# Optimization experiments

Measured on AMD Instinct MI355X. Metric: run time of the kernel, lower is better.

The kernel has to match this reference:

```python
import jax, jax.numpy as jnp
import numpy as np

N = 8192
IN_F = 512
OUT_F = 128
NEG_BIG = -9.0e15


def setup_inputs() -> dict:
    key = jax.random.key(0)
    k_x, k_adj, k_w, k_a1, k_a2 = jax.random.split(key, 5)
    X = jax.random.normal(k_x, (N, IN_F), dtype=jnp.float32)
    adj = jax.random.randint(k_adj, (N, N), 0, 2, dtype=jnp.int32)
    # xavier_uniform with gain=1.414
    gain = 1.414
    lim_w = gain * np.sqrt(6.0 / (IN_F + OUT_F))
    W = jax.random.uniform(k_w, (IN_F, OUT_F), minval=-lim_w, maxval=lim_w, dtype=jnp.float32)
    lim_a = gain * np.sqrt(6.0 / (OUT_F + 1))
    a_1 = jax.random.uniform(k_a1, (OUT_F, 1), minval=-lim_a, maxval=lim_a, dtype=jnp.float32)
    a_2 = jax.random.uniform(k_a2, (OUT_F, 1), minval=-lim_a, maxval=lim_a, dtype=jnp.float32)
    return {"X": X, "adj": adj, "W": W, "a_1": a_1, "a_2": a_2}


def reference(X, adj, W, a_1, a_2):
    h = X @ W                         # [N, out]
    Wh1 = h @ a_1                     # [N, 1]
    Wh2 = h @ a_2                     # [N, 1]
    alpha = Wh1 + Wh2.T               # [N, N] broadcast score sum
    s = jax.nn.sigmoid(alpha)
    masked = jnp.where(adj > 0, s, jnp.float32(NEG_BIG))
    attn = jax.nn.softmax(masked, axis=1)  # dropout p=0.0 -> identity
    return attn @ h                   # [N, out]
```

## Files before the change

### kernel.cpp

```cpp
#include <hip/hip_runtime.h>
#include <hip/hip_bf16.h>

#define N_NODES 8192
#define IN_F 512
#define OUT_F 128
#define KSHIFT 3
#define KP (1 << KSHIFT)
#define KT_PER (256 >> KSHIFT)
#define LOG2E 1.4426950408889634f

typedef unsigned short u16;
typedef unsigned int u32;
typedef short s16x8 __attribute__((ext_vector_type(8)));
typedef float f32x4 __attribute__((ext_vector_type(4)));
typedef u32 u32x4 __attribute__((ext_vector_type(4)));

__device__ __forceinline__ u16 f2bf(float f) {
    union { float f; unsigned u; } x; x.f = f;
    unsigned r = x.u + 0x7FFFu + ((x.u >> 16) & 1u);
    return (u16)(r >> 16);
}

__device__ __forceinline__ u32 packbf2(float a, float b) {
    __hip_bfloat162 h = __float22bfloat162_rn(make_float2(a, b));
    u32 u; __builtin_memcpy(&u, &h, 4);
    return u;
}

__device__ __forceinline__ float edge_p(float wh1, float w2, int keep) {
    float alpha = wh1 + w2;
    float e = exp2f(-LOG2E * alpha);
    float s = __builtin_amdgcn_rcpf(1.0f + e);
    float p = exp2f(LOG2E * s);
    return keep ? p : 0.0f;
}

__global__ void repack_W(const float* __restrict__ W, u16* __restrict__ W_frag) {
    int tid = blockIdx.x * 256 + threadIdx.x;
    int j = tid & 7;
    int lane = (tid >> 3) & 63;
    int nt = (tid >> 9) & 7;
    int kt = tid >> 12;
    int k = kt * 32 + (lane >> 4) * 8 + j;
    int n = nt * 16 + (lane & 15);
    W_frag[tid] = f2bf(W[k * OUT_F + n]);
}

__global__ void compute_Wa(const float* __restrict__ W, const float* __restrict__ a1,
                           const float* __restrict__ a2,
                           float* __restrict__ Wa1, float* __restrict__ Wa2) {
    int k = blockIdx.x * 256 + threadIdx.x;
    if (k >= IN_F) return;
    float s1 = 0.f, s2 = 0.f;
    #pragma unroll 8
    for (int n = 0; n < OUT_F; n++) {
        float w = W[k * OUT_F + n];
        s1 += w * a1[n];
        s2 += w * a2[n];
    }
    Wa1[k] = s1; Wa2[k] = s2;
}

__global__ __launch_bounds__(256)
void gemm_h(const float* __restrict__ X, const u16* __restrict__ W_frag,
            const float* __restrict__ Wa1, const float* __restrict__ Wa2,
            float* __restrict__ Wh1, float* __restrict__ Wh2,
            u16* __restrict__ h_frag) {
    int tid = threadIdx.x;
    int wave = tid >> 6;
    int lane = tid & 63;
    int quad = lane >> 4;
    int lid = lane & 15;
    int rbase = blockIdx.x * 16;
    const float* xrow = X + (size_t)(rbase + lid) * IN_F;
    const s16x8* Wf = (const s16x8*)W_frag;
    f32x4 acc0 = {}, acc1 = {};
    float p1 = 0.f, p2 = 0.f;
    int nt0 = wave * 2;

    for (int kt = 0; kt < 16; kt++) {
        int k0 = kt * 32 + quad * 8;
        float4 x0 = *(const float4*)(xrow + k0);
        float4 x1 = *(const float4*)(xrow + k0 + 4);
        u32x4 uv;
        uv.x = packbf2(x0.x, x0.y); uv.y = packbf2(x0.z, x0.w);
        uv.z = packbf2(x1.x, x1.y); uv.w = packbf2(x1.z, x1.w);
        s16x8 a = __builtin_bit_cast(s16x8, uv);
        if (wave == 0) {
            float4 wa = *(const float4*)(Wa1 + k0);
            float4 wb = *(const float4*)(Wa1 + k0 + 4);
            float4 wc = *(const float4*)(Wa2 + k0);
            float4 wd = *(const float4*)(Wa2 + k0 + 4);
        p1 += x0.x*wa.x + x0.y*wa.y + x0.z*wa.z + x0.w*wa.w
            + x1.x*wb.x + x1.y*wb.y + x1.z*wb.z + x1.w*wb.w;
        p2 += x0.x*wc.x + x0.y*wc.y + x0.z*wc.z + x0.w*wc.w
            + x1.x*wd.x + x1.y*wd.y + x1.z*wd.z + x1.w*wd.w;
        }
        s16x8 b0 = Wf[(kt * 8 + nt0) * 64 + lane];
        s16x8 b1 = Wf[(kt * 8 + nt0 + 1) * 64 + lane];
        acc0 = __builtin_amdgcn_mfma_f32_16x16x32_bf16(a, b0, acc0, 0, 0, 0);
        acc1 = __builtin_amdgcn_mfma_f32_16x16x32_bf16(a, b1, acc1, 0, 0, 0);
    }

    #pragma unroll
    for (int reg = 0; reg < 4; reg++) {
        int row = rbase + quad * 4 + reg;
        int ktile = row >> 5, kl = row & 31;
        int lane2 = (kl >> 3) * 16 + lid, j2 = kl & 7;
        h_frag[(size_t)((ktile * 8 + nt0) * 64 + lane2) * 8 + j2] = f2bf(acc0[reg]);
        h_frag[(size_t)((ktile * 8 + nt0 + 1) * 64 + lane2) * 8 + j2] = f2bf(acc1[reg]);
    }
    if (wave == 0) {
        p1 += __shfl_xor(p1, 16, 64); p1 += __shfl_xor(p1, 32, 64);
        p2 += __shfl_xor(p2, 16, 64); p2 += __shfl_xor(p2, 32, 64);
        if (lane < 16) { Wh1[rbase + lid] = p1; Wh2[rbase + lid] = p2; }
    }
}

__global__ __launch_bounds__(256)
void attn_kernel(const int* __restrict__ adj, const float* __restrict__ Wh1,
                 const float* __restrict__ Wh2, const u16* __restrict__ h_frag,
                 float* __restrict__ out_part, float* __restrict__ sum_part) {
    int tid = threadIdx.x;
    int wave = tid >> 6;
    int lane = tid & 63;
    int quad = lane >> 4;
    int lid = lane & 15;
    int rtile = blockIdx.x >> KSHIFT;
    int kh = blockIdx.x & (KP - 1);
    int rbase = rtile * 128 + wave * 32;
    int r0 = rbase + lid, r1 = r0 + 16;

    float wh10 = Wh1[r0], wh11 = Wh1[r1];
    f32x4 acc0[8] = {}, acc1[8] = {};
    float ps0 = 0.f, ps1 = 0.f;
    const s16x8* Hf = (const s16x8*)h_frag;
    const int* adjrow0 = adj + (size_t)r0 * N_NODES;
    const int* adjrow1 = adj + (size_t)r1 * N_NODES;

    const int kt0 = kh * KT_PER;
    #pragma unroll 1
    for (int kt = kt0; kt < kt0 + KT_PER; kt++) {
        int k0 = kt * 32 + quad * 8;
        int4 aj0a = *(const int4*)(adjrow0 + k0);
        int4 aj0b = *(const int4*)(adjrow0 + k0 + 4);
        int4 aj1a = *(const int4*)(adjrow1 + k0);
        int4 aj1b = *(const int4*)(adjrow1 + k0 + 4);
        float4 w20 = *(const float4*)(Wh2 + k0);
        float4 w21 = *(const float4*)(Wh2 + k0 + 4);

        float e0 = edge_p(wh10, w20.x, aj0a.x), e1 = edge_p(wh10, w20.y, aj0a.y);
        float e2 = edge_p(wh10, w20.z, aj0a.z), e3 = edge_p(wh10, w20.w, aj0a.w);
        float e4 = edge_p(wh10, w21.x, aj0b.x), e5 = edge_p(wh10, w21.y, aj0b.y);
        float e6 = edge_p(wh10, w21.z, aj0b.z), e7 = edge_p(wh10, w21.w, aj0b.w);
        ps0 += ((e0 + e1) + (e2 + e3)) + ((e4 + e5) + (e6 + e7));
        u32x4 uv0;
        uv0.x = packbf2(e0, e1); uv0.y = packbf2(e2, e3);
        uv0.z = packbf2(e4, e5); uv0.w = packbf2(e6, e7);

        float f0 = edge_p(wh11, w20.x, aj1a.x), f1 = edge_p(wh11, w20.y, aj1a.y);
        float f2 = edge_p(wh11, w20.z, aj1a.z), f3 = edge_p(wh11, w20.w, aj1a.w);
        float f4 = edge_p(wh11, w21.x, aj1b.x), f5 = edge_p(wh11, w21.y, aj1b.y);
        float f6 = edge_p(wh11, w21.z, aj1b.z), f7 = edge_p(wh11, w21.w, aj1b.w);
        ps1 += ((f0 + f1) + (f2 + f3)) + ((f4 + f5) + (f6 + f7));
        u32x4 uv1;
        uv1.x = packbf2(f0, f1); uv1.y = packbf2(f2, f3);
        uv1.z = packbf2(f4, f5); uv1.w = packbf2(f6, f7);

        s16x8 af0 = __builtin_bit_cast(s16x8, uv0);
        s16x8 af1 = __builtin_bit_cast(s16x8, uv1);

        #pragma unroll
        for (int nt = 0; nt < 8; nt++) {
            s16x8 b = Hf[(kt * 8 + nt) * 64 + lane];
            acc0[nt] = __builtin_amdgcn_mfma_f32_16x16x32_bf16(af0, b, acc0[nt], 0, 0, 0);
            acc1[nt] = __builtin_amdgcn_mfma_f32_16x16x32_bf16(af1, b, acc1[nt], 0, 0, 0);
        }
    }

    ps0 += __shfl_xor(ps0, 16, 64); ps0 += __shfl_xor(ps0, 32, 64);
    ps1 += __shfl_xor(ps1, 16, 64); ps1 += __shfl_xor(ps1, 32, 64);
    if (quad == 0) {
        sum_part[(size_t)kh * N_NODES + r0] = ps0;
        sum_part[(size_t)kh * N_NODES + r1] = ps1;
    }

    #pragma unroll
    for (int nt = 0; nt < 8; nt++) {
        #pragma unroll
        for (int reg = 0; reg < 4; reg++) {
            int row0 = rbase + quad * 4 + reg;
            int col = nt * 16 + lid;
            out_part[((size_t)kh * N_NODES + row0) * OUT_F + col] = acc0[nt][reg];
            out_part[((size_t)kh * N_NODES + row0 + 16) * OUT_F + col] = acc1[nt][reg];
        }
    }
}

__global__ void finalize(const float* __restrict__ out_part,
                         const float* __restrict__ sum_part,
                         float* __restrict__ out) {
    int gid = blockIdx.x * 256 + threadIdx.x;
    int i = gid >> 7;
    float s = 0.f, v = 0.f;
    for (int kh = 0; kh < KP; kh++) {
        s += sum_part[(size_t)kh * N_NODES + i];
        v += out_part[(size_t)kh * N_NODES * OUT_F + gid];
    }
    out[gid] = v / s;
}

extern "C" void kernel_launch(void* const* d_in, const int* in_sizes, int n_in,
                              void* d_out, int out_size, void* d_ws, size_t ws_size,
                              hipStream_t stream) {
    const float* X   = (const float*)d_in[0];
    const int*   adj = (const int*)d_in[1];
    const float* W   = (const float*)d_in[2];
    const float* a1  = (const float*)d_in[3];
    const float* a2  = (const float*)d_in[4];

    const size_t BASE = (size_t)4 << 20;
    char* ws = (char*)d_ws;
    float* Wh1 = (float*)(ws);
    float* Wh2 = (float*)(ws + (32 << 10));
    float* Wa1 = (float*)(ws + (64 << 10));
    float* Wa2 = (float*)(ws + (66 << 10));
    u16* W_frag = (u16*)(ws + (128 << 10));
    u16* h_frag = (u16*)(ws + (256 << 10));
    float* out_part = (float*)(ws + BASE);
    float* sum_part = (float*)(ws + BASE + ((size_t)KP << 22));
    float* out = (float*)d_out;

    hipLaunchKernelGGL(repack_W, dim3(256), dim3(256), 0, stream, W, W_frag);
    hipLaunchKernelGGL(compute_Wa, dim3(2), dim3(256), 0, stream, W, a1, a2, Wa1, Wa2);
    hipLaunchKernelGGL(gemm_h, dim3(512), dim3(256), 0, stream,
                       X, W_frag, Wa1, Wa2, Wh1, Wh2, h_frag);
    hipLaunchKernelGGL(attn_kernel, dim3(64 * KP), dim3(256), 0, stream,
                       adj, Wh1, Wh2, h_frag, out_part, sum_part);
    hipLaunchKernelGGL(finalize, dim3((N_NODES * OUT_F) / 256), dim3(256), 0, stream,
                       out_part, sum_part, out);
}
```

Before: 438.0 us.

## Stage h tiles in LDS, prefetch adjacency two steps ahead, double K split

The attention kernel now loads each group of four k-tiles of h fragments into shared memory once per block, so the four waves no longer each fetch them from global memory. It also software-prefetches the adjacency int4 loads two iterations ahead into register double buffers. The K split doubles, giving twice as many blocks with shorter loops. The price is more partial outputs to write and reduce, extra barriers, and higher register pressure.

```diff
diff --git a/kernel.cpp b/kernel.cpp
--- a/kernel.cpp
+++ b/kernel.cpp
@@ -4,7 +4,7 @@
 #define N_NODES 8192
 #define IN_F 512
 #define OUT_F 128
-#define KSHIFT 3
+#define KSHIFT 4
 #define KP (1 << KSHIFT)
 #define KT_PER (256 >> KSHIFT)
 #define LOG2E 1.4426950408889634f
@@ -91,10 +91,10 @@
             float4 wb = *(const float4*)(Wa1 + k0 + 4);
             float4 wc = *(const float4*)(Wa2 + k0);
             float4 wd = *(const float4*)(Wa2 + k0 + 4);
-        p1 += x0.x*wa.x + x0.y*wa.y + x0.z*wa.z + x0.w*wa.w
-            + x1.x*wb.x + x1.y*wb.y + x1.z*wb.z + x1.w*wb.w;
-        p2 += x0.x*wc.x + x0.y*wc.y + x0.z*wc.z + x0.w*wc.w
-            + x1.x*wd.x + x1.y*wd.y + x1.z*wd.z + x1.w*wd.w;
+            p1 += x0.x*wa.x + x0.y*wa.y + x0.z*wa.z + x0.w*wa.w
+                + x1.x*wb.x + x1.y*wb.y + x1.z*wb.z + x1.w*wb.w;
+            p2 += x0.x*wc.x + x0.y*wc.y + x0.z*wc.z + x0.w*wc.w
+                + x1.x*wd.x + x1.y*wd.y + x1.z*wd.z + x1.w*wd.w;
         }
         s16x8 b0 = Wf[(kt * 8 + nt0) * 64 + lane];
         s16x8 b1 = Wf[(kt * 8 + nt0 + 1) * 64 + lane];
@@ -121,6 +121,8 @@
 void attn_kernel(const int* __restrict__ adj, const float* __restrict__ Wh1,
                  const float* __restrict__ Wh2, const u16* __restrict__ h_frag,
                  float* __restrict__ out_part, float* __restrict__ sum_part) {
+    __shared__ s16x8 lds_h[2048];
+
     int tid = threadIdx.x;
     int wave = tid >> 6;
     int lane = tid & 63;
@@ -139,43 +141,81 @@
     const int* adjrow1 = adj + (size_t)r1 * N_NODES;
 
     const int kt0 = kh * KT_PER;
+    const int ktlast = kt0 + KT_PER - 1;
+
+    int4 P0a[2], P0b[2], P1a[2], P1b[2];
+    {
+        int ka = kt0 * 32 + quad * 8;
+        P0a[0] = *(const int4*)(adjrow0 + ka);
+        P0b[0] = *(const int4*)(adjrow0 + ka + 4);
+        P1a[0] = *(const int4*)(adjrow1 + ka);
+        P1b[0] = *(const int4*)(adjrow1 + ka + 4);
+        int kb = ka + 32;
+        P0a[1] = *(const int4*)(adjrow0 + kb);
+        P0b[1] = *(const int4*)(adjrow0 + kb + 4);
+        P1a[1] = *(const int4*)(adjrow1 + kb);
+        P1b[1] = *(const int4*)(adjrow1 + kb + 4);
+    }
+
     #pragma unroll 1
-    for (int kt = kt0; kt < kt0 + KT_PER; kt++) {
-        int k0 = kt * 32 + quad * 8;
-        int4 aj0a = *(const int4*)(adjrow0 + k0);
-        int4 aj0b = *(const int4*)(adjrow0 + k0 + 4);
-        int4 aj1a = *(const int4*)(adjrow1 + k0);
-        int4 aj1b = *(const int4*)(adjrow1 + k0 + 4);
-        float4 w20 = *(const float4*)(Wh2 + k0);
-        float4 w21 = *(const float4*)(Wh2 + k0 + 4);
-
-        float e0 = edge_p(wh10, w20.x, aj0a.x), e1 = edge_p(wh10, w20.y, aj0a.y);
-        float e2 = edge_p(wh10, w20.z, aj0a.z), e3 = edge_p(wh10, w20.w, aj0a.w);
-        float e4 = edge_p(wh10, w21.x, aj0b.x), e5 = edge_p(wh10, w21.y, aj0b.y);
-        float e6 = edge_p(wh10, w21.z, aj0b.z), e7 = edge_p(wh10, w21.w, aj0b.w);
-        ps0 += ((e0 + e1) + (e2 + e3)) + ((e4 + e5) + (e6 + e7));
-        u32x4 uv0;
-        uv0.x = packbf2(e0, e1); uv0.y = packbf2(e2, e3);
-        uv0.z = packbf2(e4, e5); uv0.w = packbf2(e6, e7);
-
-        float f0 = edge_p(wh11, w20.x, aj1a.x), f1 = edge_p(wh11, w20.y, aj1a.y);
-        float f2 = edge_p(wh11, w20.z, aj1a.z), f3 = edge_p(wh11, w20.w, aj1a.w);
-        float f4 = edge_p(wh11, w21.x, aj1b.x), f5 = edge_p(wh11, w21.y, aj1b.y);
-        float f6 = edge_p(wh11, w21.z, aj1b.z), f7 = edge_p(wh11, w21.w, aj1b.w);
-        ps1 += ((f0 + f1) + (f2 + f3)) + ((f4 + f5) + (f6 + f7));
-        u32x4 uv1;
-        uv1.x = packbf2(f0, f1); uv1.y = packbf2(f2, f3);
-        uv1.z = packbf2(f4, f5); uv1.w = packbf2(f6, f7);
-
-        s16x8 af0 = __builtin_bit_cast(s16x8, uv0);
-        s16x8 af1 = __builtin_bit_cast(s16x8, uv1);
-
-        #pragma unroll
-        for (int nt = 0; nt < 8; nt++) {
-            s16x8 b = Hf[(kt * 8 + nt) * 64 + lane];
-            acc0[nt] = __builtin_amdgcn_mfma_f32_16x16x32_bf16(af0, b, acc0[nt], 0, 0, 0);
-            acc1[nt] = __builtin_amdgcn_mfma_f32_16x16x32_bf16(af1, b, acc1[nt], 0, 0, 0);
+    for (int phase = 0; phase < 4; phase++) {
+        const s16x8* src = Hf + (size_t)(kt0 + phase * 4) * 512;
+        s16x8 t0 = src[tid],        t1 = src[256 + tid];
+        s16x8 t2 = src[512 + tid],  t3 = src[768 + tid];
+        s16x8 t4 = src[1024 + tid], t5 = src[1280 + tid];
+        s16x8 t6 = src[1536 + tid], t7 = src[1792 + tid];
+        lds_h[tid] = t0;        lds_h[256 + tid] = t1;
+        lds_h[512 + tid] = t2;  lds_h[768 + tid] = t3;
+        lds_h[1024 + tid] = t4; lds_h[1280 + tid] = t5;
+        lds_h[1536 + tid] = t6; lds_h[1792 + tid] = t7;
+        __syncthreads();
+
+        #pragma unroll 1
+        for (int ktl = 0; ktl < 4; ktl++) {
+            int kt = kt0 + phase * 4 + ktl;
+            int slot = kt & 1;
+            int4 aj0a = P0a[slot], aj0b = P0b[slot];
+            int4 aj1a = P1a[slot], aj1b = P1b[slot];
+            int ktn = (kt + 2 <= ktlast) ? (kt + 2) : ktlast;
+            int kn = ktn * 32 + quad * 8;
+            P0a[slot] = *(const int4*)(adjrow0 + kn);
+            P0b[slot] = *(const int4*)(adjrow0 + kn + 4);
+            P1a[slot] = *(const int4*)(adjrow1 + kn);
+            P1b[slot] = *(const int4*)(adjrow1 + kn + 4);
+
+            int k0 = kt * 32 + quad * 8;
+            float4 w20 = *(const float4*)(Wh2 + k0);
+            float4 w21 = *(const float4*)(Wh2 + k0 + 4);
+
+            float e0 = edge_p(wh10, w20.x, aj0a.x), e1 = edge_p(wh10, w20.y, aj0a.y);
+            float e2 = edge_p(wh10, w20.z, aj0a.z), e3 = edge_p(wh10, w20.w, aj0a.w);
+            float e4 = edge_p(wh10, w21.x, aj0b.x), e5 = edge_p(wh10, w21.y, aj0b.y);
+            float e6 = edge_p(wh10, w21.z, aj0b.z), e7 = edge_p(wh10, w21.w, aj0b.w);
+            ps0 += ((e0 + e1) + (e2 + e3)) + ((e4 + e5) + (e6 + e7));
+            u32x4 uv0;
+            uv0.x = packbf2(e0, e1); uv0.y = packbf2(e2, e3);
+            uv0.z = packbf2(e4, e5); uv0.w = packbf2(e6, e7);
+
+            float f0 = edge_p(wh11, w20.x, aj1a.x), f1 = edge_p(wh11, w20.y, aj1a.y);
+            float f2 = edge_p(wh11, w20.z, aj1a.z), f3 = edge_p(wh11, w20.w, aj1a.w);
+            float f4 = edge_p(wh11, w21.x, aj1b.x), f5 = edge_p(wh11, w21.y, aj1b.y);
+            float f6 = edge_p(wh11, w21.z, aj1b.z), f7 = edge_p(wh11, w21.w, aj1b.w);
+            ps1 += ((f0 + f1) + (f2 + f3)) + ((f4 + f5) + (f6 + f7));
+            u32x4 uv1;
+            uv1.x = packbf2(f0, f1); uv1.y = packbf2(f2, f3);
+            uv1.z = packbf2(f4, f5); uv1.w = packbf2(f6, f7);
+
+            s16x8 af0 = __builtin_bit_cast(s16x8, uv0);
+            s16x8 af1 = __builtin_bit_cast(s16x8, uv1);
+
+            #pragma unroll
+            for (int nt = 0; nt < 8; nt++) {
+                s16x8 b = lds_h[(ktl * 8 + nt) * 64 + lane];
+                acc0[nt] = __builtin_amdgcn_mfma_f32_16x16x32_bf16(af0, b, acc0[nt], 0, 0, 0);
+                acc1[nt] = __builtin_amdgcn_mfma_f32_16x16x32_bf16(af1, b, acc1[nt], 0, 0, 0);
+            }
         }
+        __syncthreads();
     }
 
     ps0 += __shfl_xor(ps0, 16, 64); ps0 += __shfl_xor(ps0, 32, 64);
```

Result: slower. 475.6 us (+8.6%).
